# Kernel optimization log

Measured on AMD Instinct MI355X. Metric: run time of the kernel, lower is better.

Reference implementation:

```python
import jax, jax.numpy as jnp
import numpy as np

B, S, D = 8, 1024, 768
H = 12
DH = D // H
MLP = 3072
PATCHES = 1024  # query rows >= PATCHES//2 get their scores zeroed pre-softmax
EPS = 1e-6


def setup_inputs() -> dict:
    key = jax.random.key(0)
    ks = jax.random.split(key, 16)
    s = lambda fan_in: 1.0 / np.sqrt(fan_in)
    inp = {
        "x": jax.random.normal(ks[0], (B, S, D), dtype=jnp.float32),
        "Wq": jax.random.normal(ks[1], (D, D), dtype=jnp.float32) * s(D),
        "bq": jnp.zeros((D,), jnp.float32),
        "Wk": jax.random.normal(ks[2], (D, D), dtype=jnp.float32) * s(D),
        "bk": jnp.zeros((D,), jnp.float32),
        "Wv": jax.random.normal(ks[3], (D, D), dtype=jnp.float32) * s(D),
        "bv": jnp.zeros((D,), jnp.float32),
        "Wo": jax.random.normal(ks[4], (D, D), dtype=jnp.float32) * s(D),
        "bo": jnp.zeros((D,), jnp.float32),
        "ln1_g": jnp.ones((D,), jnp.float32),
        "ln1_b": jnp.zeros((D,), jnp.float32),
        "ln2_g": jnp.ones((D,), jnp.float32),
        "ln2_b": jnp.zeros((D,), jnp.float32),
        "W1": jax.random.normal(ks[5], (D, MLP), dtype=jnp.float32) * s(D),
        "b1": jax.random.normal(ks[6], (MLP,), dtype=jnp.float32) * 1e-6,
        "W2": jax.random.normal(ks[7], (MLP, D), dtype=jnp.float32) * s(MLP),
        "b2": jax.random.normal(ks[8], (D,), dtype=jnp.float32) * 1e-6,
    }
    return inp


def _layernorm(x, g, b):
    mu = jnp.mean(x, axis=-1, keepdims=True)
    var = jnp.var(x, axis=-1, keepdims=True)
    return (x - mu) * jax.lax.rsqrt(var + EPS) * g + b


def reference(x, Wq, bq, Wk, bk, Wv, bv, Wo, bo, ln1_g, ln1_b, ln2_g, ln2_b, W1, b1, W2, b2):
    h = x
    xn = _layernorm(x, ln1_g, ln1_b)
    # QKV projections -> [B, H, S, DH]
    q = (xn @ Wq + bq).reshape(B, S, H, DH).transpose(0, 2, 1, 3)
    k = (xn @ Wk + bk).reshape(B, S, H, DH).transpose(0, 2, 1, 3)
    v = (xn @ Wv + bv).reshape(B, S, H, DH).transpose(0, 2, 1, 3)
    scores = jnp.einsum("bhqd,bhkd->bhqk", q, k) / np.sqrt(DH).astype(np.float32)
    # zero scores for query rows >= PATCHES//2 (softmax of zeros -> uniform attn)
    row_keep = (jnp.arange(S) < PATCHES // 2)[None, None, :, None]
    scores = jnp.where(row_keep, scores, 0.0)
    probs = jax.nn.softmax(scores, axis=-1)
    ctx = jnp.einsum("bhqk,bhkd->bhqd", probs, v)
    ctx = ctx.transpose(0, 2, 1, 3).reshape(B, S, D)
    attn_out = ctx @ Wo + bo
    x = attn_out + h
    h = x
    xn = _layernorm(x, ln2_g, ln2_b)
    x = jax.nn.relu(xn @ W1 + b1) @ W2 + b2
    x = x + h
    return x
```

## Files before the change

kernel.cpp:

```cpp
#include <hip/hip_runtime.h>
#include <hip/hip_bf16.h>

#define SDIM 1024
#define DDIM 768
#define HEADS 12
#define DHD 64
#define MLPD 3072
#define BSZ 8

typedef unsigned short u16;
typedef unsigned int u32;
typedef __attribute__((ext_vector_type(8))) short short8;
typedef __attribute__((ext_vector_type(4))) float f32x4;
typedef __attribute__((ext_vector_type(4))) u16 u16x4;
typedef __attribute__((ext_vector_type(4))) float float4x;

__device__ __forceinline__ u16 f2b(float f) {
  u32 u = __float_as_uint(f);
  u = (u + 0x7fffu + ((u >> 16) & 1u)) >> 16;
  return (u16)u;
}
__device__ __forceinline__ float b2f(u16 u) {
  return __uint_as_float(((u32)u) << 16);
}

#define GLDS16(g, l)                                                        \
  __builtin_amdgcn_global_load_lds(                                         \
      (const __attribute__((address_space(1))) unsigned int*)(g),           \
      (__attribute__((address_space(3))) unsigned int*)(l), 16, 0, 0)

__global__ __launch_bounds__(256) void transpose_w(const float* __restrict__ src,
                                                   u16* __restrict__ dst,
                                                   int K, int N) {
  __shared__ float tile[32][33];
  const int tx = threadIdx.x & 31, ty = threadIdx.x >> 5;
  const int n0 = blockIdx.x * 32, k0 = blockIdx.y * 32;
#pragma unroll
  for (int i = 0; i < 4; ++i)
    tile[ty + i * 8][tx] = src[(size_t)(k0 + ty + i * 8) * N + n0 + tx];
  __syncthreads();
#pragma unroll
  for (int i = 0; i < 4; ++i)
    dst[(size_t)(n0 + ty + i * 8) * K + k0 + tx] = f2b(tile[tx][ty + i * 8]);
}

__global__ void bias_concat(const float* __restrict__ bq, const float* __restrict__ bk,
                            const float* __restrict__ bv, float* __restrict__ dst) {
  int i = blockIdx.x * 256 + threadIdx.x;
  if (i < 3 * DDIM)
    dst[i] = (i < DDIM) ? bq[i] : (i < 2 * DDIM) ? bk[i - DDIM] : bv[i - 2 * DDIM];
}

__global__ __launch_bounds__(256) void ln_kernel(const float* __restrict__ x,
                                                 const float* __restrict__ g,
                                                 const float* __restrict__ b,
                                                 u16* __restrict__ y) {
  const int row = blockIdx.x * 4 + (threadIdx.x >> 6);
  const int lane = threadIdx.x & 63;
  const float4x* xp = (const float4x*)(x + (size_t)row * DDIM);
  float4x v[3];
  float sum = 0.f, sq = 0.f;
#pragma unroll
  for (int i = 0; i < 3; ++i) {
    v[i] = xp[lane + i * 64];
#pragma unroll
    for (int j = 0; j < 4; ++j) { sum += v[i][j]; sq += v[i][j] * v[i][j]; }
  }
#pragma unroll
  for (int m = 1; m < 64; m <<= 1) {
    sum += __shfl_xor(sum, m, 64);
    sq  += __shfl_xor(sq, m, 64);
  }
  const float mu = sum * (1.f / DDIM);
  const float var = sq * (1.f / DDIM) - mu * mu;
  const float rstd = rsqrtf(var + 1e-6f);
  const float4x* gp = (const float4x*)g;
  const float4x* bp = (const float4x*)b;
  u16x4* yp = (u16x4*)(y + (size_t)row * DDIM);
#pragma unroll
  for (int i = 0; i < 3; ++i) {
    float4x gg = gp[lane + i * 64], bb = bp[lane + i * 64];
    u16x4 o;
#pragma unroll
    for (int j = 0; j < 4; ++j) o[j] = f2b((v[i][j] - mu) * rstd * gg[j] + bb[j]);
    yp[lane + i * 64] = o;
  }
}

template <int EP>
__global__ __launch_bounds__(256) void gemm_bf16(
    const u16* __restrict__ A, const u16* __restrict__ Bt,
    int M, int N, int K,
    const float* __restrict__ bias, const float* __restrict__ res,
    float* __restrict__ outF, u16* __restrict__ o0, u16* __restrict__ o1,
    u16* __restrict__ o2) {
  __shared__ u16 As[128 * 32];
  __shared__ u16 Bs[128 * 32];
  const int tid = threadIdx.x;
  const int lane = tid & 63, wid = tid >> 6;
  const int l15 = lane & 15, lg = lane >> 4;
  const int wm = wid >> 1, wn = wid & 1;
  const int m0 = blockIdx.x * 128, n0 = blockIdx.y * 128;

  const u16* ag = A + (size_t)(m0 + (tid >> 2)) * K + (tid & 3) * 8;
  const u16* bg = Bt + (size_t)(n0 + (tid >> 2)) * K + (tid & 3) * 8;
  u16* lA = As + tid * 8;
  u16* lB = Bs + tid * 8;
  const size_t half = (size_t)64 * K;

  f32x4 acc[4][4] = {};

  for (int k0 = 0; k0 < K; k0 += 32) {
    __syncthreads();
    GLDS16(ag + k0, lA);
    GLDS16(ag + half + k0, lA + 2048);
    GLDS16(bg + k0, lB);
    GLDS16(bg + half + k0, lB + 2048);
    __syncthreads();
    short8 af[4], bfr[4];
#pragma unroll
    for (int i = 0; i < 4; ++i)
      af[i] = *(const short8*)&As[(wm * 64 + i * 16 + l15) * 32 + 8 * lg];
#pragma unroll
    for (int i = 0; i < 4; ++i)
      bfr[i] = *(const short8*)&Bs[(wn * 64 + i * 16 + l15) * 32 + 8 * lg];
#pragma unroll
    for (int im = 0; im < 4; ++im)
#pragma unroll
      for (int in = 0; in < 4; ++in)
        acc[im][in] = __builtin_amdgcn_mfma_f32_16x16x32_bf16(af[im], bfr[in], acc[im][in], 0, 0, 0);
  }

#pragma unroll
  for (int im = 0; im < 4; ++im) {
#pragma unroll
    for (int in = 0; in < 4; ++in) {
      const int gn = n0 + wn * 64 + in * 16 + l15;
#pragma unroll
      for (int r = 0; r < 4; ++r) {
        const int gm = m0 + wm * 64 + im * 16 + lg * 4 + r;
        float v = acc[im][in][r];
        if (EP == 0) {
          v += bias[gn];
          const int sel = gn / DDIM;
          const int d = gn - sel * DDIM;
          const int h = d >> 6, dh = d & 63;
          const int bb = gm >> 10, ss = gm & 1023;
          const u16 bv = f2b(v);
          const int bhid = bb * HEADS + h;
          if (sel == 0)      o0[((size_t)bhid * SDIM + ss) * DHD + dh] = bv;
          else if (sel == 1) o1[((size_t)bhid * SDIM + ss) * DHD + dh] = bv;
          else               o2[((size_t)bhid * DHD + dh) * SDIM + ss] = bv;
        } else if (EP == 1) {
          const size_t idx = (size_t)gm * N + gn;
          outF[idx] = v + bias[gn] + res[idx];
        } else {
          const size_t idx = (size_t)gm * N + gn;
          o0[idx] = f2b(fmaxf(v + bias[gn], 0.f));
        }
      }
    }
  }
}

__global__ __launch_bounds__(256) void attn_kernel(const u16* __restrict__ Q,
                                                   const u16* __restrict__ Km,
                                                   const u16* __restrict__ Vt,
                                                   u16* __restrict__ ctx) {
  __shared__ u16 Ks[2][4096];
  __shared__ u16 Vs[2][4096];
  __shared__ u16 P_lds[4][16][72];
  const int bh = blockIdx.y;
  const int tid = threadIdx.x;
  const int wid = tid >> 6, lane = tid & 63;
  const int l15 = lane & 15, lg = lane >> 4;
  const int q0 = blockIdx.x * 64 + wid * 16;

  const u16* Qp = Q + (size_t)bh * SDIM * DHD;
  const char* Kp = (const char*)(Km + (size_t)bh * SDIM * DHD);
  const char* Vp = (const char*)(Vt + (size_t)bh * DHD * SDIM);

  int so[2], vo_base[2], ldso[2];
#pragma unroll
  for (int j = 0; j < 2; ++j) {
    const int o = j * 4096 + tid * 16;
    const int row = o >> 7;
    ldso[j] = o;
    so[j] = o ^ ((row & 7) << 4);
    vo_base[j] = row * 2048 + ((o & 127) ^ ((row & 7) << 4));
  }

  short8 aq0 = *(const short8*)&Qp[(q0 + l15) * DHD + 8 * lg];
  short8 aq1 = *(const short8*)&Qp[(q0 + l15) * DHD + 32 + 8 * lg];

  float mrow[4], lrow[4];
  f32x4 o_acc[4] = {};
#pragma unroll
  for (int r = 0; r < 4; ++r) { mrow[r] = -1e30f; lrow[r] = 0.f; }

#pragma unroll
  for (int j = 0; j < 2; ++j) {
    GLDS16(Kp + so[j], (char*)&Ks[0][0] + ldso[j]);
    GLDS16(Vp + vo_base[j], (char*)&Vs[0][0] + ldso[j]);
  }

  for (int kb = 0; kb < 16; ++kb) {
    const int cur = kb & 1;
    if (kb < 15) {
#pragma unroll
      for (int j = 0; j < 2; ++j) {
        GLDS16(Kp + (size_t)(kb + 1) * 8192 + so[j], (char*)&Ks[cur ^ 1][0] + ldso[j]);
        GLDS16(Vp + (size_t)(kb + 1) * 128 + vo_base[j], (char*)&Vs[cur ^ 1][0] + ldso[j]);
      }
      asm volatile("s_waitcnt vmcnt(4)" ::: "memory");
    } else {
      asm volatile("s_waitcnt vmcnt(0)" ::: "memory");
    }
    __builtin_amdgcn_s_barrier();
    __builtin_amdgcn_sched_barrier(0);

    f32x4 s_acc[4] = {};
#pragma unroll
    for (int in = 0; in < 4; ++in) {
      const int row = in * 16 + l15;
      const int a0 = (row * 128 + lg * 16) ^ ((row & 7) << 4);
      const int a1 = (row * 128 + 64 + lg * 16) ^ ((row & 7) << 4);
      short8 b0 = *(const short8*)((const char*)&Ks[cur][0] + a0);
      short8 b1 = *(const short8*)((const char*)&Ks[cur][0] + a1);
      s_acc[in] = __builtin_amdgcn_mfma_f32_16x16x32_bf16(aq0, b0, s_acc[in], 0, 0, 0);
      s_acc[in] = __builtin_amdgcn_mfma_f32_16x16x32_bf16(aq1, b1, s_acc[in], 0, 0, 0);
    }
#pragma unroll
    for (int in = 0; in < 4; ++in)
#pragma unroll
      for (int r = 0; r < 4; ++r) s_acc[in][r] *= 0.125f;

    float alpha[4], rsum[4];
#pragma unroll
    for (int r = 0; r < 4; ++r) {
      float v = -1e30f;
#pragma unroll
      for (int in = 0; in < 4; ++in) v = fmaxf(v, s_acc[in][r]);
#pragma unroll
      for (int m = 1; m < 16; m <<= 1) v = fmaxf(v, __shfl_xor(v, m, 64));
      const float mn = fmaxf(mrow[r], v);
      alpha[r] = __expf(mrow[r] - mn);
      mrow[r] = mn;
      rsum[r] = 0.f;
    }
#pragma unroll
    for (int in = 0; in < 4; ++in)
#pragma unroll
      for (int r = 0; r < 4; ++r) {
        const float p = __expf(s_acc[in][r] - mrow[r]);
        rsum[r] += p;
        P_lds[wid][lg * 4 + r][in * 16 + l15] = f2b(p);
      }
#pragma unroll
    for (int r = 0; r < 4; ++r) {
      float v = rsum[r];
#pragma unroll
      for (int m = 1; m < 16; m <<= 1) v += __shfl_xor(v, m, 64);
      lrow[r] = lrow[r] * alpha[r] + v;
    }
#pragma unroll
    for (int in = 0; in < 4; ++in)
#pragma unroll
      for (int r = 0; r < 4; ++r) o_acc[in][r] *= alpha[r];

    short8 ap0 = *(const short8*)&P_lds[wid][l15][8 * lg];
    short8 ap1 = *(const short8*)&P_lds[wid][l15][32 + 8 * lg];

#pragma unroll
    for (int in = 0; in < 4; ++in) {
      const int row = in * 16 + l15;
      const int a0 = (row * 128 + lg * 16) ^ ((row & 7) << 4);
      const int a1 = (row * 128 + 64 + lg * 16) ^ ((row & 7) << 4);
      short8 b0 = *(const short8*)((const char*)&Vs[cur][0] + a0);
      short8 b1 = *(const short8*)((const char*)&Vs[cur][0] + a1);
      o_acc[in] = __builtin_amdgcn_mfma_f32_16x16x32_bf16(ap0, b0, o_acc[in], 0, 0, 0);
      o_acc[in] = __builtin_amdgcn_mfma_f32_16x16x32_bf16(ap1, b1, o_acc[in], 0, 0, 0);
    }
    __builtin_amdgcn_sched_barrier(0);
    __builtin_amdgcn_s_barrier();
    __builtin_amdgcn_sched_barrier(0);
  }

  const int bb = bh / HEADS, h = bh - bb * HEADS;
#pragma unroll
  for (int in = 0; in < 4; ++in)
#pragma unroll
    for (int r = 0; r < 4; ++r) {
      const int s = q0 + lg * 4 + r;
      const float v = o_acc[in][r] / lrow[r];
      ctx[((size_t)(bb * SDIM + s)) * DDIM + h * 64 + in * 16 + l15] = f2b(v);
    }
}

__global__ __launch_bounds__(256) void meanv_kernel(const u16* __restrict__ Vt,
                                                    u16* __restrict__ ctx) {
  __shared__ float mean_s[64];
  const int bh = blockIdx.x;
  const int t = threadIdx.x;
  const int dh = t >> 2, part = t & 3;
  const u16* vp = Vt + (size_t)bh * DHD * SDIM + (size_t)dh * SDIM + part * 256;
  float s = 0.f;
#pragma unroll
  for (int i = 0; i < 32; ++i) {
    short8 v = *(const short8*)&vp[i * 8];
#pragma unroll
    for (int j = 0; j < 8; ++j) s += b2f((u16)v[j]);
  }
  s += __shfl_xor(s, 1, 64);
  s += __shfl_xor(s, 2, 64);
  if (part == 0) mean_s[dh] = s * (1.f / 1024.f);
  __syncthreads();
  const int b = bh / HEADS, h = bh - b * HEADS;
  u16x4 val;
#pragma unroll
  for (int j = 0; j < 4; ++j) val[j] = f2b(mean_s[(t & 15) * 4 + j]);
#pragma unroll
  for (int i = 0; i < 32; ++i) {
    const int row = 512 + i * 16 + (t >> 4);
    *(u16x4*)&ctx[((size_t)(b * SDIM + row)) * DDIM + h * 64 + (t & 15) * 4] = val;
  }
}

extern "C" void kernel_launch(void* const* d_in, const int* in_sizes, int n_in,
                              void* d_out, int out_size, void* d_ws, size_t ws_size,
                              hipStream_t stream) {
  const float* x    = (const float*)d_in[0];
  const float* Wq   = (const float*)d_in[1];
  const float* bq   = (const float*)d_in[2];
  const float* Wk   = (const float*)d_in[3];
  const float* bk   = (const float*)d_in[4];
  const float* Wv   = (const float*)d_in[5];
  const float* bv   = (const float*)d_in[6];
  const float* Wo   = (const float*)d_in[7];
  const float* bo   = (const float*)d_in[8];
  const float* ln1g = (const float*)d_in[9];
  const float* ln1b = (const float*)d_in[10];
  const float* ln2g = (const float*)d_in[11];
  const float* ln2b = (const float*)d_in[12];
  const float* W1   = (const float*)d_in[13];
  const float* b1   = (const float*)d_in[14];
  const float* W2   = (const float*)d_in[15];
  const float* b2   = (const float*)d_in[16];

  char* ws = (char*)d_ws;
  u16* xn1   = (u16*)(ws + 0);
  u16* qb    = (u16*)(ws + 12582912);
  u16* kbuf  = (u16*)(ws + 25165824);
  u16* vtb   = (u16*)(ws + 37748736);
  u16* h1    = (u16*)(ws + 0);
  u16* ctx   = (u16*)(ws + 50331648);
  float* x2  = (float*)(ws + 62914560);
  u16* xn2   = (u16*)(ws + 88080384);
  u16* wqkvT = (u16*)(ws + 100663296);
  u16* woT   = (u16*)(ws + 104202240);
  u16* w1T   = (u16*)(ws + 105381888);
  u16* w2T   = (u16*)(ws + 110100480);
  float* bqkv = (float*)(ws + 114819072);

  transpose_w<<<dim3(24, 24), 256, 0, stream>>>(Wq, wqkvT, 768, 768);
  transpose_w<<<dim3(24, 24), 256, 0, stream>>>(Wk, wqkvT + 768 * 768, 768, 768);
  transpose_w<<<dim3(24, 24), 256, 0, stream>>>(Wv, wqkvT + 2 * 768 * 768, 768, 768);
  transpose_w<<<dim3(24, 24), 256, 0, stream>>>(Wo, woT, 768, 768);
  transpose_w<<<dim3(96, 24), 256, 0, stream>>>(W1, w1T, 768, 3072);
  transpose_w<<<dim3(24, 96), 256, 0, stream>>>(W2, w2T, 3072, 768);
  bias_concat<<<9, 256, 0, stream>>>(bq, bk, bv, bqkv);

  ln_kernel<<<2048, 256, 0, stream>>>(x, ln1g, ln1b, xn1);
  gemm_bf16<0><<<dim3(64, 18), 256, 0, stream>>>(xn1, wqkvT, 8192, 2304, 768,
                                                 bqkv, nullptr, nullptr, qb, kbuf, vtb);
  attn_kernel<<<dim3(8, 96), 256, 0, stream>>>(qb, kbuf, vtb, ctx);
  meanv_kernel<<<96, 256, 0, stream>>>(vtb, ctx);
  gemm_bf16<1><<<dim3(64, 6), 256, 0, stream>>>(ctx, woT, 8192, 768, 768,
                                                bo, x, x2, nullptr, nullptr, nullptr);
  ln_kernel<<<2048, 256, 0, stream>>>(x2, ln2g, ln2b, xn2);
  gemm_bf16<2><<<dim3(64, 24), 256, 0, stream>>>(xn2, w1T, 8192, 3072, 768,
                                                 b1, nullptr, nullptr, h1, nullptr, nullptr);
  gemm_bf16<1><<<dim3(64, 6), 256, 0, stream>>>(h1, w2T, 8192, 768, 3072,
                                                b2, x2, (float*)d_out, nullptr, nullptr, nullptr);
}
```

Baseline: 411.6 us.

## Double-buffer GEMM LDS tiles with BK=64 and XOR-swizzled layout

Rewrites the bf16 GEMM main loop so that global-to-LDS loads for the next 64-wide K tile are issued into a second LDS buffer while MFMAs run on the current one. Synchronisation uses manual vmcnt waits and raw barriers instead of a pair of __syncthreads per step. The LDS layout gains an XOR swizzle on 16-byte chunks to avoid bank conflicts on the fragment reads, and MFMA issue priority is raised. This costs four times the LDS (64 KB per block), which may lower occupancy, and the hand-written waitcnt counts must be correct.

Measured after the change: 385.4 us. -6.4%, faster.

```diff
diff --git a/kernel.cpp b/kernel.cpp
--- a/kernel.cpp
+++ b/kernel.cpp
@@ -94,41 +94,73 @@
     const float* __restrict__ bias, const float* __restrict__ res,
     float* __restrict__ outF, u16* __restrict__ o0, u16* __restrict__ o1,
     u16* __restrict__ o2) {
-  __shared__ u16 As[128 * 32];
-  __shared__ u16 Bs[128 * 32];
+  __shared__ u16 As[2][128 * 64];
+  __shared__ u16 Bs[2][128 * 64];
   const int tid = threadIdx.x;
   const int lane = tid & 63, wid = tid >> 6;
   const int l15 = lane & 15, lg = lane >> 4;
   const int wm = wid >> 1, wn = wid & 1;
   const int m0 = blockIdx.x * 128, n0 = blockIdx.y * 128;
 
-  const u16* ag = A + (size_t)(m0 + (tid >> 2)) * K + (tid & 3) * 8;
-  const u16* bg = Bt + (size_t)(n0 + (tid >> 2)) * K + (tid & 3) * 8;
-  u16* lA = As + tid * 8;
-  u16* lB = Bs + tid * 8;
-  const size_t half = (size_t)64 * K;
+  const int srow = tid >> 3;
+  const int scb = ((tid & 7) << 4) ^ ((srow & 7) << 4);
+  const u16* ag = A + (size_t)(m0 + srow) * K + (scb >> 1);
+  const u16* bg = Bt + (size_t)(n0 + srow) * K + (scb >> 1);
 
   f32x4 acc[4][4] = {};
-
-  for (int k0 = 0; k0 < K; k0 += 32) {
-    __syncthreads();
-    GLDS16(ag + k0, lA);
-    GLDS16(ag + half + k0, lA + 2048);
-    GLDS16(bg + k0, lB);
-    GLDS16(bg + half + k0, lB + 2048);
-    __syncthreads();
-    short8 af[4], bfr[4];
-#pragma unroll
-    for (int i = 0; i < 4; ++i)
-      af[i] = *(const short8*)&As[(wm * 64 + i * 16 + l15) * 32 + 8 * lg];
-#pragma unroll
-    for (int i = 0; i < 4; ++i)
-      bfr[i] = *(const short8*)&Bs[(wn * 64 + i * 16 + l15) * 32 + 8 * lg];
-#pragma unroll
-    for (int im = 0; im < 4; ++im)
-#pragma unroll
-      for (int in = 0; in < 4; ++in)
-        acc[im][in] = __builtin_amdgcn_mfma_f32_16x16x32_bf16(af[im], bfr[in], acc[im][in], 0, 0, 0);
+  const int NT = K >> 6;
+
+#define STAGE_G(buf, koff)                                                    \
+  {                                                                           \
+    _Pragma("unroll") for (int j = 0; j < 4; ++j)                             \
+        GLDS16(ag + (koff) + (size_t)j * 32 * K, &As[buf][tid * 8 + j * 2048]); \
+    _Pragma("unroll") for (int j = 0; j < 4; ++j)                             \
+        GLDS16(bg + (koff) + (size_t)j * 32 * K, &Bs[buf][tid * 8 + j * 2048]); \
+  }
+
+  STAGE_G(0, 0);
+  int cur = 0;
+  for (int t = 0; t < NT; ++t) {
+    if (t + 1 < NT) {
+      STAGE_G(cur ^ 1, (t + 1) * 64);
+      asm volatile("s_waitcnt vmcnt(8)" ::: "memory");
+    } else {
+      asm volatile("s_waitcnt vmcnt(0)" ::: "memory");
+    }
+    __builtin_amdgcn_s_barrier();
+    __builtin_amdgcn_sched_barrier(0);
+    const char* ab = (const char*)As[cur];
+    const char* bb = (const char*)Bs[cur];
+    short8 af[4][2], bf[4][2];
+#pragma unroll
+    for (int i = 0; i < 4; ++i) {
+      const int row = wm * 64 + i * 16 + l15;
+      const int rx = (l15 & 7) << 4;
+#pragma unroll
+      for (int kk = 0; kk < 2; ++kk)
+        af[i][kk] = *(const short8*)(ab + row * 128 + ((kk * 64 + lg * 16) ^ rx));
+    }
+#pragma unroll
+    for (int i = 0; i < 4; ++i) {
+      const int row = wn * 64 + i * 16 + l15;
+      const int rx = (l15 & 7) << 4;
+#pragma unroll
+      for (int kk = 0; kk < 2; ++kk)
+        bf[i][kk] = *(const short8*)(bb + row * 128 + ((kk * 64 + lg * 16) ^ rx));
+    }
+    __builtin_amdgcn_s_setprio(1);
+#pragma unroll
+    for (int kk = 0; kk < 2; ++kk)
+#pragma unroll
+      for (int im = 0; im < 4; ++im)
+#pragma unroll
+        for (int in = 0; in < 4; ++in)
+          acc[im][in] = __builtin_amdgcn_mfma_f32_16x16x32_bf16(af[im][kk], bf[in][kk],
+                                                                acc[im][in], 0, 0, 0);
+    __builtin_amdgcn_s_setprio(0);
+    __builtin_amdgcn_sched_barrier(0);
+    __builtin_amdgcn_s_barrier();
+    cur ^= 1;
   }
 
 #pragma unroll
@@ -145,9 +177,9 @@
           const int sel = gn / DDIM;
           const int d = gn - sel * DDIM;
           const int h = d >> 6, dh = d & 63;
-          const int bb = gm >> 10, ss = gm & 1023;
+          const int bb2 = gm >> 10, ss = gm & 1023;
           const u16 bv = f2b(v);
-          const int bhid = bb * HEADS + h;
+          const int bhid = bb2 * HEADS + h;
           if (sel == 0)      o0[((size_t)bhid * SDIM + ss) * DHD + dh] = bv;
           else if (sel == 1) o1[((size_t)bhid * SDIM + ss) * DHD + dh] = bv;
           else               o2[((size_t)bhid * DHD + dh) * SDIM + ss] = bv;
```

## Double-buffer GEMM A tiles in LDS with swizzle and direct-register B loads

Applied to the files above, without the earlier changes.

Rewrites the bf16 GEMM main loop to use a BK=64 double-buffered LDS pipeline for A, with an XOR swizzle on the LDS layout to avoid bank conflicts. B fragments are loaded straight from global memory into registers and double-buffered there, which drops B from LDS. The loop uses explicit waitcnt and barriers plus MFMA priority raising so loads overlap with compute, and K becomes a template constant. The cost is higher register pressure and hand-tuned waitcnt counts that must match the number of loads in flight.

After: 503.1 us. 1.22x slower.

```diff
diff --git a/kernel.cpp b/kernel.cpp
--- a/kernel.cpp
+++ b/kernel.cpp
@@ -87,49 +87,94 @@
   }
 }
 
-template <int EP>
+template <int EP, int KDIM>
 __global__ __launch_bounds__(256) void gemm_bf16(
-    const u16* __restrict__ A, const u16* __restrict__ Bt,
-    int M, int N, int K,
+    const u16* __restrict__ A, const u16* __restrict__ Bt, int N,
     const float* __restrict__ bias, const float* __restrict__ res,
     float* __restrict__ outF, u16* __restrict__ o0, u16* __restrict__ o1,
     u16* __restrict__ o2) {
-  __shared__ u16 As[128 * 32];
-  __shared__ u16 Bs[128 * 32];
+  __shared__ u16 As[2][128 * 64];
   const int tid = threadIdx.x;
   const int lane = tid & 63, wid = tid >> 6;
   const int l15 = lane & 15, lg = lane >> 4;
   const int wm = wid >> 1, wn = wid & 1;
   const int m0 = blockIdx.x * 128, n0 = blockIdx.y * 128;
 
-  const u16* ag = A + (size_t)(m0 + (tid >> 2)) * K + (tid & 3) * 8;
-  const u16* bg = Bt + (size_t)(n0 + (tid >> 2)) * K + (tid & 3) * 8;
-  u16* lA = As + tid * 8;
-  u16* lB = Bs + tid * 8;
-  const size_t half = (size_t)64 * K;
+  const int srow = tid >> 3;
+  const int scb = ((tid & 7) << 4) ^ ((srow & 7) << 4);
+  const u16* ag = A + (size_t)(m0 + srow) * KDIM + (scb >> 1);
+  const u16* bp = Bt + (size_t)(n0 + wn * 64 + l15) * KDIM + lg * 8;
 
   f32x4 acc[4][4] = {};
-
-  for (int k0 = 0; k0 < K; k0 += 32) {
-    __syncthreads();
-    GLDS16(ag + k0, lA);
-    GLDS16(ag + half + k0, lA + 2048);
-    GLDS16(bg + k0, lB);
-    GLDS16(bg + half + k0, lB + 2048);
-    __syncthreads();
-    short8 af[4], bfr[4];
-#pragma unroll
-    for (int i = 0; i < 4; ++i)
-      af[i] = *(const short8*)&As[(wm * 64 + i * 16 + l15) * 32 + 8 * lg];
-#pragma unroll
-    for (int i = 0; i < 4; ++i)
-      bfr[i] = *(const short8*)&Bs[(wn * 64 + i * 16 + l15) * 32 + 8 * lg];
-#pragma unroll
-    for (int im = 0; im < 4; ++im)
-#pragma unroll
-      for (int in = 0; in < 4; ++in)
-        acc[im][in] = __builtin_amdgcn_mfma_f32_16x16x32_bf16(af[im], bfr[in], acc[im][in], 0, 0, 0);
-  }
+  constexpr int NT = KDIM >> 6;
+
+#define STAGE_A(buf, t)                                                      \
+  { _Pragma("unroll") for (int j = 0; j < 4; ++j)                            \
+        GLDS16(ag + (t) * 64 + (size_t)j * 32 * KDIM,                        \
+               &As[buf][tid * 8 + j * 2048]); }
+
+#define LOADB(B, t)                                                          \
+  { _Pragma("unroll") for (int in = 0; in < 4; ++in)                         \
+        _Pragma("unroll") for (int kk = 0; kk < 2; ++kk)                     \
+            B[in][kk] = *(const short8*)(bp + (size_t)in * 16 * KDIM +       \
+                                         (t) * 64 + kk * 32); }
+
+#define READA(buf)                                                           \
+  { _Pragma("unroll") for (int i = 0; i < 4; ++i) {                          \
+      const int row = wm * 64 + i * 16 + l15;                                \
+      const int rx = (l15 & 7) << 4;                                         \
+      _Pragma("unroll") for (int kk = 0; kk < 2; ++kk)                       \
+          af[i][kk] = *(const short8*)((const char*)As[buf] + row * 128 +    \
+                                       ((kk * 64 + lg * 16) ^ rx));          \
+    } }
+
+#define MFMA_ALL(B)                                                          \
+  { __builtin_amdgcn_s_setprio(1);                                           \
+    _Pragma("unroll") for (int kk = 0; kk < 2; ++kk)                         \
+        _Pragma("unroll") for (int im = 0; im < 4; ++im)                     \
+            _Pragma("unroll") for (int in = 0; in < 4; ++in)                 \
+                acc[im][in] = __builtin_amdgcn_mfma_f32_16x16x32_bf16(       \
+                    af[im][kk], B[in][kk], acc[im][in], 0, 0, 0);            \
+    __builtin_amdgcn_s_setprio(0); }
+
+  short8 B0[4][2], B1[4][2], af[4][2];
+  STAGE_A(0, 0);
+  LOADB(B0, 0);
+
+  for (int t = 0; t < NT; t += 2) {
+    STAGE_A(1, t + 1);
+    LOADB(B1, t + 1);
+    __builtin_amdgcn_sched_barrier(0);
+    asm volatile("s_waitcnt vmcnt(12)" ::: "memory");
+    __builtin_amdgcn_s_barrier();
+    __builtin_amdgcn_sched_barrier(0);
+    READA(0);
+    asm volatile("s_waitcnt lgkmcnt(0)" ::: "memory");
+    __builtin_amdgcn_sched_barrier(0);
+    __builtin_amdgcn_s_barrier();
+    MFMA_ALL(B0);
+
+    if (t + 2 < NT) {
+      STAGE_A(0, t + 2);
+      LOADB(B0, t + 2);
+      __builtin_amdgcn_sched_barrier(0);
+      asm volatile("s_waitcnt vmcnt(12)" ::: "memory");
+    } else {
+      asm volatile("s_waitcnt vmcnt(0)" ::: "memory");
+    }
+    __builtin_amdgcn_s_barrier();
+    __builtin_amdgcn_sched_barrier(0);
+    READA(1);
+    asm volatile("s_waitcnt lgkmcnt(0)" ::: "memory");
+    __builtin_amdgcn_sched_barrier(0);
+    __builtin_amdgcn_s_barrier();
+    MFMA_ALL(B1);
+  }
+
+#undef STAGE_A
+#undef LOADB
+#undef READA
+#undef MFMA_ALL
 
 #pragma unroll
   for (int im = 0; im < 4; ++im) {
@@ -139,24 +184,22 @@
 #pragma unroll
       for (int r = 0; r < 4; ++r) {
         const int gm = m0 + wm * 64 + im * 16 + lg * 4 + r;
-        float v = acc[im][in][r];
+        float v = acc[im][in][r] + bias[gn];
         if (EP == 0) {
-          v += bias[gn];
           const int sel = gn / DDIM;
           const int d = gn - sel * DDIM;
           const int h = d >> 6, dh = d & 63;
-          const int bb = gm >> 10, ss = gm & 1023;
+          const int bb2 = gm >> 10, ss = gm & 1023;
           const u16 bv = f2b(v);
-          const int bhid = bb * HEADS + h;
+          const int bhid = bb2 * HEADS + h;
           if (sel == 0)      o0[((size_t)bhid * SDIM + ss) * DHD + dh] = bv;
           else if (sel == 1) o1[((size_t)bhid * SDIM + ss) * DHD + dh] = bv;
           else               o2[((size_t)bhid * DHD + dh) * SDIM + ss] = bv;
         } else if (EP == 1) {
           const size_t idx = (size_t)gm * N + gn;
-          outF[idx] = v + bias[gn] + res[idx];
+          outF[idx] = v + res[idx];
         } else {
-          const size_t idx = (size_t)gm * N + gn;
-          o0[idx] = f2b(fmaxf(v + bias[gn], 0.f));
+          o0[(size_t)gm * N + gn] = f2b(fmaxf(v, 0.f));
         }
       }
     }
@@ -371,15 +414,15 @@
   bias_concat<<<9, 256, 0, stream>>>(bq, bk, bv, bqkv);
 
   ln_kernel<<<2048, 256, 0, stream>>>(x, ln1g, ln1b, xn1);
-  gemm_bf16<0><<<dim3(64, 18), 256, 0, stream>>>(xn1, wqkvT, 8192, 2304, 768,
-                                                 bqkv, nullptr, nullptr, qb, kbuf, vtb);
+  gemm_bf16<0, 768><<<dim3(64, 18), 256, 0, stream>>>(xn1, wqkvT, 2304,
+                                                      bqkv, nullptr, nullptr, qb, kbuf, vtb);
   attn_kernel<<<dim3(8, 96), 256, 0, stream>>>(qb, kbuf, vtb, ctx);
   meanv_kernel<<<96, 256, 0, stream>>>(vtb, ctx);
-  gemm_bf16<1><<<dim3(64, 6), 256, 0, stream>>>(ctx, woT, 8192, 768, 768,
-                                                bo, x, x2, nullptr, nullptr, nullptr);
+  gemm_bf16<1, 768><<<dim3(64, 6), 256, 0, stream>>>(ctx, woT, 768,
+                                                     bo, x, x2, nullptr, nullptr, nullptr);
   ln_kernel<<<2048, 256, 0, stream>>>(x2, ln2g, ln2b, xn2);
-  gemm_bf16<2><<<dim3(64, 24), 256, 0, stream>>>(xn2, w1T, 8192, 3072, 768,
-                                                 b1, nullptr, nullptr, h1, nullptr, nullptr);
-  gemm_bf16<1><<<dim3(64, 6), 256, 0, stream>>>(h1, w2T, 8192, 768, 3072,
-                                                b2, x2, (float*)d_out, nullptr, nullptr, nullptr);
-}
+  gemm_bf16<2, 768><<<dim3(64, 24), 256, 0, stream>>>(xn2, w1T, 3072,
+                                                      b1, nullptr, nullptr, h1, nullptr, nullptr);
+  gemm_bf16<1, 3072><<<dim3(64, 6), 256, 0, stream>>>(h1, w2T, 768,
+                                                      b2, x2, (float*)d_out, nullptr, nullptr, nullptr);
+}
```
